# Optimization experiments

Measured on AMD Instinct MI355X. Metric: run time of the kernel, lower is better.

The kernel has to match this reference:

```python
import jax, jax.numpy as jnp
import numpy as np

PAD_IDX = 1
NEG_BIG = jnp.float32(-1e18)


def setup_inputs() -> dict:
    key = jax.random.key(0)
    ks = jax.random.split(key, 7)
    B, L, K, D, V, C = 64, 350, 8, 300, 50000, 20
    node_sets = jax.random.randint(ks[0], (B, L), 0, V, dtype=jnp.int64)
    embedded_node = jax.random.normal(ks[1], (B, L, D), dtype=jnp.float32)
    edge_weight = jax.random.uniform(ks[2], (B, L, K), dtype=jnp.float32)
    embedded_neighbor_node = jax.random.normal(ks[3], (B, L, K, D), dtype=jnp.float32)
    information_rate = jax.random.uniform(ks[4], (V, 1), dtype=jnp.float32)
    W = jax.random.normal(ks[5], (C, D), dtype=jnp.float32) * 0.05
    b = jax.random.normal(ks[6], (C,), dtype=jnp.float32) * 0.05
    return {"node_sets": node_sets, "embedded_node": embedded_node,
            "edge_weight": edge_weight,
            "embedded_neighbor_node": embedded_neighbor_node,
            "information_rate": information_rate, "W": W, "b": b}


def reference(node_sets, embedded_node, edge_weight, embedded_neighbor_node,
              information_rate, W, b):
    # weighted neighbor messages: [B,L,K,D]
    tmp = edge_weight[..., None] * embedded_neighbor_node
    # masked_fill(tmp == 0, -1e18); dropout_rate=0 -> identity
    tmp = jnp.where(tmp == 0, NEG_BIG, tmp)
    # max-pool over neighbors K -> [B,L,D]
    M = tmp.max(axis=2)
    # gather per-node information rate [B,L,1]; padding nodes forced to 1
    ir = information_rate[node_sets]
    ir = jnp.where((node_sets == PAD_IDX)[..., None], jnp.float32(1.0), ir)
    # gated combine, sum over nodes L -> [B,D]
    combined = (1.0 - ir) * M + ir * embedded_node
    s = combined.sum(axis=1)
    # linear + relu + softmax -> [B,C]
    x = jax.nn.relu(jnp.einsum('bd,cd->bc', s, W) + b)
    return jax.nn.softmax(x, axis=1)
```

## Files before the change

### kernel.cpp

```cpp
#include <hip/hip_runtime.h>
#include <math.h>

#define Bn 64
#define Ln 350
#define Kn 8
#define Dn 300
#define Cn 20
#define SPLIT 16
#define PAD_IDX 1
#define NEG_BIG (-1e18f)

typedef float v4f __attribute__((ext_vector_type(4)));

template <bool PARTIAL>
__global__ __launch_bounds__(256) void mp_reduce(
    const int* __restrict__ node_sets,
    const float* __restrict__ emb_node,
    const float* __restrict__ edge_w,
    const float* __restrict__ emb_nbr,
    const float* __restrict__ info_rate,
    float* __restrict__ ws)
{
    __shared__ __align__(16) float sAcc[4][Dn + 4];

    const int bid  = blockIdx.x;
    const int b    = bid / SPLIT;
    const int sidx = bid % SPLIT;
    const int tid  = threadIdx.x;
    const int wave = tid >> 6;
    const int lane = tid & 63;
    const bool has1 = (lane < (Dn / 4 - 64));
    const int q0 = 4 * lane;
    const int q1 = 256 + 4 * lane;

    v4f acc0 = (v4f)(0.f);
    v4f acc1 = (v4f)(0.f);

    for (int j = wave;; j += 4) {
        const int l = sidx + j * SPLIT;
        if (l >= Ln) break;
        const size_t row = (size_t)b * Ln + l;

        const float* ewp = edge_w + row * Kn;
        const v4f ew0 = *reinterpret_cast<const v4f*>(ewp);
        const v4f ew1 = *reinterpret_cast<const v4f*>(ewp + 4);
        const float ewv[Kn] = {ew0.x, ew0.y, ew0.z, ew0.w, ew1.x, ew1.y, ew1.z, ew1.w};

        const int node = node_sets[row];
        const float ir = (node == PAD_IDX) ? 1.0f : info_rate[node];
        const float om = 1.0f - ir;

        const float* nb = emb_nbr + row * (size_t)(Kn * Dn);
        const float* en = emb_node + row * (size_t)Dn;

        {
            v4f m = (v4f)(NEG_BIG);
            #pragma unroll
            for (int k = 0; k < Kn; ++k) {
                const v4f v = *reinterpret_cast<const v4f*>(nb + k * Dn + q0);
                const float w = ewv[k];
                float x0 = w * v.x, x1 = w * v.y, x2 = w * v.z, x3 = w * v.w;
                x0 = (x0 == 0.f) ? NEG_BIG : x0;
                x1 = (x1 == 0.f) ? NEG_BIG : x1;
                x2 = (x2 == 0.f) ? NEG_BIG : x2;
                x3 = (x3 == 0.f) ? NEG_BIG : x3;
                m.x = fmaxf(m.x, x0);
                m.y = fmaxf(m.y, x1);
                m.z = fmaxf(m.z, x2);
                m.w = fmaxf(m.w, x3);
            }
            const v4f e = *reinterpret_cast<const v4f*>(en + q0);
            acc0.x += om * m.x + ir * e.x;
            acc0.y += om * m.y + ir * e.y;
            acc0.z += om * m.z + ir * e.z;
            acc0.w += om * m.w + ir * e.w;
        }

        if (has1) {
            v4f m = (v4f)(NEG_BIG);
            #pragma unroll
            for (int k = 0; k < Kn; ++k) {
                const v4f v = *reinterpret_cast<const v4f*>(nb + k * Dn + q1);
                const float w = ewv[k];
                float x0 = w * v.x, x1 = w * v.y, x2 = w * v.z, x3 = w * v.w;
                x0 = (x0 == 0.f) ? NEG_BIG : x0;
                x1 = (x1 == 0.f) ? NEG_BIG : x1;
                x2 = (x2 == 0.f) ? NEG_BIG : x2;
                x3 = (x3 == 0.f) ? NEG_BIG : x3;
                m.x = fmaxf(m.x, x0);
                m.y = fmaxf(m.y, x1);
                m.z = fmaxf(m.z, x2);
                m.w = fmaxf(m.w, x3);
            }
            const v4f e = *reinterpret_cast<const v4f*>(en + q1);
            acc1.x += om * m.x + ir * e.x;
            acc1.y += om * m.y + ir * e.y;
            acc1.z += om * m.z + ir * e.z;
            acc1.w += om * m.w + ir * e.w;
        }
    }

    *reinterpret_cast<v4f*>(&sAcc[wave][q0]) = acc0;
    if (has1) *reinterpret_cast<v4f*>(&sAcc[wave][q1]) = acc1;
    __syncthreads();

    if (PARTIAL) {
        float* dst = ws + (size_t)bid * Dn;
        for (int d = tid; d < Dn; d += 256)
            dst[d] = sAcc[0][d] + sAcc[1][d] + sAcc[2][d] + sAcc[3][d];
    } else {
        for (int d = tid; d < Dn; d += 256) {
            const float sum = sAcc[0][d] + sAcc[1][d] + sAcc[2][d] + sAcc[3][d];
            atomicAdd(&ws[b * Dn + d], sum);
        }
    }
}

template <int NPART>
__global__ __launch_bounds__(256) void mp_head(
    const float* __restrict__ part,
    const float* __restrict__ Wm,
    const float* __restrict__ bias,
    float* __restrict__ out)
{
    __shared__ __align__(16) float wsum[4][Dn + 4];
    __shared__ __align__(16) float ssh[Dn + 4];
    __shared__ float xsh[Cn];

    const int b = blockIdx.x;
    const int t = threadIdx.x;
    const int wave = t >> 6;
    const int lane = t & 63;
    const bool has1 = (lane < (Dn / 4 - 64));
    const int q0 = 4 * lane;
    const int q1 = 256 + 4 * lane;

    if (NPART >= 4) {
        constexpr int PPW = (NPART >= 4) ? NPART / 4 : 1;
        v4f a0 = (v4f)(0.f), a1 = (v4f)(0.f);
        #pragma unroll
        for (int p = 0; p < PPW; ++p) {
            const float* src = part + ((size_t)b * NPART + wave * PPW + p) * Dn;
            a0 += *reinterpret_cast<const v4f*>(src + q0);
            if (has1) a1 += *reinterpret_cast<const v4f*>(src + q1);
        }
        *reinterpret_cast<v4f*>(&wsum[wave][q0]) = a0;
        if (has1) *reinterpret_cast<v4f*>(&wsum[wave][q1]) = a1;
        __syncthreads();

        for (int d = t; d < Dn; d += 256)
            ssh[d] = wsum[0][d] + wsum[1][d] + wsum[2][d] + wsum[3][d];
    } else {
        for (int d = t; d < Dn; d += 256) ssh[d] = part[(size_t)b * Dn + d];
    }
    __syncthreads();

    for (int c = wave; c < Cn; c += 4) {
        const float* wr = Wm + (size_t)c * Dn;
        float acc = 0.f;
        {
            const v4f wv = *reinterpret_cast<const v4f*>(wr + q0);
            const v4f sv = *reinterpret_cast<const v4f*>(&ssh[q0]);
            acc += wv.x * sv.x + wv.y * sv.y + wv.z * sv.z + wv.w * sv.w;
        }
        if (has1) {
            const v4f wv = *reinterpret_cast<const v4f*>(wr + q1);
            const v4f sv = *reinterpret_cast<const v4f*>(&ssh[q1]);
            acc += wv.x * sv.x + wv.y * sv.y + wv.z * sv.z + wv.w * sv.w;
        }
        #pragma unroll
        for (int off = 32; off >= 1; off >>= 1)
            acc += __shfl_xor(acc, off, 64);
        if (lane == 0) xsh[c] = fmaxf(acc + bias[c], 0.f);
    }
    __syncthreads();

    if (t < Cn) {
        float mx = xsh[0];
        #pragma unroll
        for (int i = 1; i < Cn; ++i) mx = fmaxf(mx, xsh[i]);
        float sum = 0.f;
        #pragma unroll
        for (int i = 0; i < Cn; ++i) sum += expf(xsh[i] - mx);
        out[b * Cn + t] = expf(xsh[t] - mx) / sum;
    }
}

extern "C" void kernel_launch(void* const* d_in, const int* in_sizes, int n_in,
                              void* d_out, int out_size, void* d_ws, size_t ws_size,
                              hipStream_t stream) {
    const int*   node_sets = (const int*)d_in[0];
    const float* emb_node  = (const float*)d_in[1];
    const float* edge_w    = (const float*)d_in[2];
    const float* emb_nbr   = (const float*)d_in[3];
    const float* info_rate = (const float*)d_in[4];
    const float* Wm        = (const float*)d_in[5];
    const float* bias      = (const float*)d_in[6];
    float* out  = (float*)d_out;
    float* ws   = (float*)d_ws;

    const size_t need = (size_t)Bn * SPLIT * Dn * sizeof(float);
    if (ws_size >= need) {
        mp_reduce<true><<<dim3(Bn * SPLIT), 256, 0, stream>>>(
            node_sets, emb_node, edge_w, emb_nbr, info_rate, ws);
        mp_head<SPLIT><<<dim3(Bn), 256, 0, stream>>>(ws, Wm, bias, out);
    } else {
        hipMemsetAsync(d_ws, 0, (size_t)Bn * Dn * sizeof(float), stream);
        mp_reduce<false><<<dim3(Bn * SPLIT), 256, 0, stream>>>(
            node_sets, emb_node, edge_w, emb_nbr, info_rate, ws);
        mp_head<1><<<dim3(Bn), 256, 0, stream>>>(ws, Wm, bias, out);
    }
}
```

Measured before the change: 49.49 us.

## Fuse reduction and head into one kernel with last-block-done counter

Merges the partial-reduction kernel and the linear/softmax head into one kernel. Each block atomically adds its partial sums into a per-batch accumulator, and the last block to arrive, found through an atomic counter, computes the head. This removes the second kernel launch and the round trip through per-split partial buffers, but adds a memset, float atomics whose order is nondeterministic, and threadfence overhead.

New measurement: 178.2 us. 260% more time.

```diff
diff --git a/kernel.cpp b/kernel.cpp
--- a/kernel.cpp
+++ b/kernel.cpp
@@ -12,16 +12,21 @@
 
 typedef float v4f __attribute__((ext_vector_type(4)));
 
-template <bool PARTIAL>
-__global__ __launch_bounds__(256) void mp_reduce(
+__global__ __launch_bounds__(256) void mp_fused(
     const int* __restrict__ node_sets,
     const float* __restrict__ emb_node,
     const float* __restrict__ edge_w,
     const float* __restrict__ emb_nbr,
     const float* __restrict__ info_rate,
-    float* __restrict__ ws)
+    const float* __restrict__ Wm,
+    const float* __restrict__ bias,
+    float* __restrict__ s_acc,
+    unsigned* __restrict__ counter,
+    float* __restrict__ out)
 {
     __shared__ __align__(16) float sAcc[4][Dn + 4];
+    __shared__ float xsh[Cn];
+    __shared__ unsigned winner;
 
     const int bid  = blockIdx.x;
     const int b    = bid / SPLIT;
@@ -104,55 +109,22 @@
     if (has1) *reinterpret_cast<v4f*>(&sAcc[wave][q1]) = acc1;
     __syncthreads();
 
-    if (PARTIAL) {
-        float* dst = ws + (size_t)bid * Dn;
-        for (int d = tid; d < Dn; d += 256)
-            dst[d] = sAcc[0][d] + sAcc[1][d] + sAcc[2][d] + sAcc[3][d];
-    } else {
-        for (int d = tid; d < Dn; d += 256) {
-            const float sum = sAcc[0][d] + sAcc[1][d] + sAcc[2][d] + sAcc[3][d];
-            atomicAdd(&ws[b * Dn + d], sum);
-        }
+    for (int d = tid; d < Dn; d += 256) {
+        const float sum = sAcc[0][d] + sAcc[1][d] + sAcc[2][d] + sAcc[3][d];
+        atomicAdd(&s_acc[b * Dn + d], sum);
     }
-}
 
-template <int NPART>
-__global__ __launch_bounds__(256) void mp_head(
-    const float* __restrict__ part,
-    const float* __restrict__ Wm,
-    const float* __restrict__ bias,
-    float* __restrict__ out)
-{
-    __shared__ __align__(16) float wsum[4][Dn + 4];
-    __shared__ __align__(16) float ssh[Dn + 4];
-    __shared__ float xsh[Cn];
+    __threadfence();
+    if (tid == 0) winner = atomicAdd(&counter[b], 1u);
+    __syncthreads();
+    if (winner != SPLIT - 1) return;
 
-    const int b = blockIdx.x;
-    const int t = threadIdx.x;
-    const int wave = t >> 6;
-    const int lane = t & 63;
-    const bool has1 = (lane < (Dn / 4 - 64));
-    const int q0 = 4 * lane;
-    const int q1 = 256 + 4 * lane;
+    __threadfence();
 
-    if (NPART >= 4) {
-        constexpr int PPW = (NPART >= 4) ? NPART / 4 : 1;
-        v4f a0 = (v4f)(0.f), a1 = (v4f)(0.f);
-        #pragma unroll
-        for (int p = 0; p < PPW; ++p) {
-            const float* src = part + ((size_t)b * NPART + wave * PPW + p) * Dn;
-            a0 += *reinterpret_cast<const v4f*>(src + q0);
-            if (has1) a1 += *reinterpret_cast<const v4f*>(src + q1);
-        }
-        *reinterpret_cast<v4f*>(&wsum[wave][q0]) = a0;
-        if (has1) *reinterpret_cast<v4f*>(&wsum[wave][q1]) = a1;
-        __syncthreads();
-
-        for (int d = t; d < Dn; d += 256)
-            ssh[d] = wsum[0][d] + wsum[1][d] + wsum[2][d] + wsum[3][d];
-    } else {
-        for (int d = t; d < Dn; d += 256) ssh[d] = part[(size_t)b * Dn + d];
-    }
+    float* ssh = &sAcc[0][0];
+    for (int d = tid; d < Dn; d += 256)
+        ssh[d] = __hip_atomic_load(&s_acc[b * Dn + d],
+                                   __ATOMIC_RELAXED, __HIP_MEMORY_SCOPE_AGENT);
     __syncthreads();
 
     for (int c = wave; c < Cn; c += 4) {
@@ -175,14 +147,14 @@
     }
     __syncthreads();
 
-    if (t < Cn) {
+    if (tid < Cn) {
         float mx = xsh[0];
         #pragma unroll
         for (int i = 1; i < Cn; ++i) mx = fmaxf(mx, xsh[i]);
         float sum = 0.f;
         #pragma unroll
         for (int i = 0; i < Cn; ++i) sum += expf(xsh[i] - mx);
-        out[b * Cn + t] = expf(xsh[t] - mx) / sum;
+        out[b * Cn + tid] = expf(xsh[tid] - mx) / sum;
     }
 }
 
@@ -196,18 +168,15 @@
     const float* info_rate = (const float*)d_in[4];
     const float* Wm        = (const float*)d_in[5];
     const float* bias      = (const float*)d_in[6];
-    float* out  = (float*)d_out;
-    float* ws   = (float*)d_ws;
+    float* out = (float*)d_out;
 
-    const size_t need = (size_t)Bn * SPLIT * Dn * sizeof(float);
-    if (ws_size >= need) {
-        mp_reduce<true><<<dim3(Bn * SPLIT), 256, 0, stream>>>(
-            node_sets, emb_node, edge_w, emb_nbr, info_rate, ws);
-        mp_head<SPLIT><<<dim3(Bn), 256, 0, stream>>>(ws, Wm, bias, out);
-    } else {
-        hipMemsetAsync(d_ws, 0, (size_t)Bn * Dn * sizeof(float), stream);
-        mp_reduce<false><<<dim3(Bn * SPLIT), 256, 0, stream>>>(
-            node_sets, emb_node, edge_w, emb_nbr, info_rate, ws);
-        mp_head<1><<<dim3(Bn), 256, 0, stream>>>(ws, Wm, bias, out);
-    }
+    float*    s_acc   = (float*)d_ws;
+    unsigned* counter = (unsigned*)(s_acc + Bn * Dn);
+    const size_t zero_bytes = (size_t)Bn * Dn * sizeof(float) + Bn * sizeof(unsigned);
+
+    hipMemsetAsync(d_ws, 0, zero_bytes, stream);
+
+    mp_fused<<<dim3(Bn * SPLIT), 256, 0, stream>>>(
+        node_sets, emb_node, edge_w, emb_nbr, info_rate, Wm, bias,
+        s_acc, counter, out);
 }
```
